# Optimization experiments

Measured on AMD Instinct MI355X. Metric: run time of the kernel, lower is better.

## Reference

```python
import jax, jax.numpy as jnp
import numpy as np

N0, N1, N2 = 120000, 40000, 10000   # sampled node counts per hop
E0, E1 = 600000, 150000             # edges per block (fanout ~15)
DIN, DH, NC = 128, 256, 47


def _glorot(k, fan_in, fan_out):
    s = (2.0 / (fan_in + fan_out)) ** 0.5
    return jax.random.normal(k, (fan_in, fan_out), jnp.float32) * s


def setup_inputs() -> dict:
    key = jax.random.key(0)
    ks = jax.random.split(key, 20)
    x0 = jax.random.normal(ks[0], (N0, DIN), jnp.float32)
    src0 = jax.random.randint(ks[1], (E0,), 0, N0)
    dst0 = jax.random.randint(ks[2], (E0,), 0, N1)
    src1 = jax.random.randint(ks[3], (E1,), 0, N1)
    dst1 = jax.random.randint(ks[4], (E1,), 0, N2)
    srcb0 = jax.random.randint(ks[5], (E0,), 0, N0)
    dstb0 = jax.random.randint(ks[6], (E0,), 0, N1)
    srcb1 = jax.random.randint(ks[7], (E1,), 0, N1)
    dstb1 = jax.random.randint(ks[8], (E1,), 0, N2)
    # id_old_value_new: must satisfy idx[:n] < n for every truncation length n,
    # i.e. idx[k] in [0, k+1)
    rng = np.random.default_rng(0)
    idx = jnp.asarray((rng.random(N0) * (np.arange(N0) + 1)).astype(np.int64))
    mix_ratio = jnp.float32(0.5)
    Wl0 = _glorot(ks[9], DIN, DH); Wr0 = _glorot(ks[10], DIN, DH)
    b0 = jnp.zeros((DH,), jnp.float32)
    Wl1 = _glorot(ks[11], DH, DH); Wr1 = _glorot(ks[12], DH, DH)
    b1 = jnp.zeros((DH,), jnp.float32)
    Wlin = _glorot(ks[13], DH, NC)
    blin = jnp.zeros((NC,), jnp.float32)
    return dict(x0=x0, src0=src0, dst0=dst0, src1=src1, dst1=dst1,
                srcb0=srcb0, dstb0=dstb0, srcb1=srcb1, dstb1=dstb1,
                idx=idx, mix_ratio=mix_ratio,
                Wl0=Wl0, Wr0=Wr0, b0=b0, Wl1=Wl1, Wr1=Wr1, b1=b1,
                Wlin=Wlin, blin=blin)


def _sage(x_all, root_x, src, dst, n_root, Wl, Wr, b):
    # PyG-style SAGEConv, mean aggregation: lin_l(mean_j x_j) + lin_r(root)
    msgs = x_all[src]                                        # [E, D] gather
    s = jax.ops.segment_sum(msgs, dst, num_segments=n_root)  # [n_root, D]
    cnt = jax.ops.segment_sum(jnp.ones_like(dst, dtype=x_all.dtype), dst,
                              num_segments=n_root)
    mean = s / jnp.maximum(cnt, 1.0)[:, None]
    return mean @ Wl + root_x @ Wr + b


def reference(x0, src0, dst0, src1, dst1, srcb0, dstb0, srcb1, dstb1,
              idx, mix_ratio, Wl0, Wr0, b0, Wl1, Wr1, b1, Wlin, blin):
    blocks = [(src0, dst0, N1), (src1, dst1, N2)]
    blocks_b = [(srcb0, dstb0, N1), (srcb1, dstb1, N2)]
    params = [(Wl0, Wr0, b0), (Wl1, Wr1, b1)]
    m = mix_ratio

    # first branch (dropout omitted: inference mode)
    aggr_xs = [x0]
    for i in range(2):
        src, dst, n_root = blocks[i]
        Wl, Wr, b = params[i]
        root_x = aggr_xs[-1][:n_root]
        x = jax.nn.relu(_sage(aggr_xs[-1], root_x, src, dst, n_root, Wl, Wr, b))
        aggr_xs.append(x)

    # permuted branch via id_old_value_new gather
    aggr_xs_b = [x[idx[: x.shape[0]]] for x in aggr_xs]

    x_mix = aggr_xs[0] * m + aggr_xs_b[0] * (1.0 - m)
    for i in range(2):
        src, dst, n_root = blocks[i]
        srcb, dstb, n_root_b = blocks_b[i]
        Wl, Wr, b = params[i]
        x_new = jax.nn.relu(_sage(aggr_xs[i], x_mix[:n_root], src, dst,
                                  n_root, Wl, Wr, b))
        x_new_b = jax.nn.relu(_sage(aggr_xs_b[i], x_mix[:n_root_b], srcb, dstb,
                                    n_root_b, Wl, Wr, b))
        x_mix = x_new * m + x_new_b * (1.0 - m)

    logits = x_mix @ Wlin + blin
    return jax.nn.log_softmax(logits, axis=-1)
```

## Files before the change

kernel.cpp:

```cpp
#include <hip/hip_runtime.h>
#include <math.h>

#define N1C 40000
#define N2C 10000
#define DIN 128
#define DH  256
#define NC  47

#define TOTCNT (2 * N1C + 2 * N2C)
#define CAP 64
#define CURSTR 16

typedef __attribute__((ext_vector_type(8))) short v8s;
typedef __attribute__((ext_vector_type(4))) float v4f;
typedef __attribute__((ext_vector_type(2))) float v2f;

#if __has_builtin(__builtin_amdgcn_cvt_pk_f32_fp8)
#define HW_FP8 1
#endif

__device__ __forceinline__ unsigned short f2bf(float f) {
    unsigned int u = __float_as_uint(f);
    u += 0x7FFF + ((u >> 16) & 1);
    return (unsigned short)(u >> 16);
}
__device__ __forceinline__ float bf2f(unsigned int h) {
    return __uint_as_float(h << 16);
}

__device__ __forceinline__ unsigned char f2e4m3(float f) {
    unsigned int u = __float_as_uint(f);
    unsigned char s = (unsigned char)((u >> 24) & 0x80);
    float a = __uint_as_float(u & 0x7FFFFFFF);
    if (a > 448.0f) a = 448.0f;
    if (a < 0.015625f) {
        int k = (int)rintf(a * 512.0f);
        return s | (unsigned char)k;
    }
    unsigned int bits = __float_as_uint(a);
    int et = (int)(bits >> 23) - 127 + 7;
    unsigned int m32 = bits & 0x7FFFFF;
    unsigned int m3 = m32 >> 20;
    unsigned int rest = m32 & 0xFFFFF;
    if (rest > 0x80000 || (rest == 0x80000 && (m3 & 1))) m3++;
    if (m3 == 8) { m3 = 0; et++; }
    if (et > 15 || (et == 15 && m3 == 7)) return s | 0x7E;
    return s | (unsigned char)((et << 3) | m3);
}

__device__ __forceinline__ void dec4(unsigned int u, float& f0, float& f1,
                                     float& f2, float& f3) {
#ifdef HW_FP8
    v2f lo = __builtin_amdgcn_cvt_pk_f32_fp8((int)u, false);
    v2f hi = __builtin_amdgcn_cvt_pk_f32_fp8((int)u, true);
    f0 = lo[0]; f1 = lo[1]; f2 = hi[0]; f3 = hi[1];
#else
    auto d1 = [](unsigned int b) -> float {
        int e = (b >> 3) & 15, mm = b & 7;
        float d = (e == 0) ? (float)mm * (1.0f / 512.0f)
                           : (1.0f + (float)mm * 0.125f) * exp2f((float)(e - 7));
        return (b & 0x80) ? -d : d;
    };
    f0 = d1(u & 0xFF); f1 = d1((u >> 8) & 0xFF);
    f2 = d1((u >> 16) & 0xFF); f3 = d1(u >> 24);
#endif
}

__global__ __launch_bounds__(256) void front_fused(
        const int* __restrict__ src0, const int* __restrict__ dst0,
        const int* __restrict__ srcb0, const int* __restrict__ dstb0,
        const int* __restrict__ src1, const int* __restrict__ dst1,
        const int* __restrict__ srcb1, const int* __restrict__ dstb1,
        const int* __restrict__ perm, int* __restrict__ cur,
        int* __restrict__ bucket, int E0, int E1, int nbFill,
        const float* __restrict__ x0, unsigned char* __restrict__ x0f,
        long n8, int nbConv,
        const float* __restrict__ Wl0, const float* __restrict__ Wr0,
        const float* __restrict__ Wl1, const float* __restrict__ Wr1,
        unsigned short* __restrict__ Wt0l, unsigned short* __restrict__ Wt0r,
        unsigned short* __restrict__ Wt1l, unsigned short* __restrict__ Wt1r) {
    int b = blockIdx.x, t = threadIdx.x;
    if (b < nbFill) {
        int e = b * 256 + t;
        int tot = 2 * E0 + 2 * E1;
        if (e >= tot) return;
        int s, bin;
        if (e < E0) {
            s = src0[e];                  bin = dst0[e];
        } else if (e < 2 * E0) {
            int le = e - E0;
            s = perm[srcb0[le]];          bin = N1C + dstb0[le];
        } else if (e < 2 * E0 + E1) {
            int le = e - 2 * E0;
            s = src1[le];                 bin = 2 * N1C + dst1[le];
        } else {
            int le = e - 2 * E0 - E1;
            s = perm[srcb1[le]];          bin = 2 * N1C + N2C + dstb1[le];
        }
        int pos = atomicAdd(&cur[(size_t)bin * CURSTR], 1);
        if (pos < CAP) bucket[(size_t)bin * CAP + pos] = s;
    } else if (b < nbFill + nbConv) {
        long i = (long)(b - nbFill) * 256 + t;
        if (i >= n8) return;
        const float4* p = (const float4*)(x0 + i * 8);
        float4 a = p[0], c = p[1];
        float f[8] = {a.x, a.y, a.z, a.w, c.x, c.y, c.z, c.w};
        unsigned int q0 = 0, q1 = 0;
#pragma unroll
        for (int j = 0; j < 8; j++) {
            unsigned int e8 = f2e4m3(f[j]);
            if (j < 4) q0 |= e8 << (8 * j); else q1 |= e8 << (8 * (j - 4));
        }
        uint2 q = {q0, q1};
        *(uint2*)(x0f + i * 8) = q;
    } else {
        int id = (b - nbFill - nbConv) * 256 + t;
        const int S0 = DIN * DH;
        const int S1 = DH * DH;
        const float* W; unsigned short* Wt; int K, loc;
        if (id < S0)                   { W = Wl0; Wt = Wt0l; K = DIN; loc = id; }
        else if (id < 2 * S0)          { W = Wr0; Wt = Wt0r; K = DIN; loc = id - S0; }
        else if (id < 2 * S0 + S1)     { W = Wl1; Wt = Wt1l; K = DH;  loc = id - 2 * S0; }
        else if (id < 2 * S0 + 2 * S1) { W = Wr1; Wt = Wt1r; K = DH;  loc = id - 2 * S0 - S1; }
        else return;
        int n = loc / K, k = loc - n * K;
        Wt[(size_t)n * K + k] = f2bf(W[(size_t)k * DH + n]);
    }
}

__global__ __launch_bounds__(256) void gather_mean_128f(
        const unsigned char* __restrict__ xf, const int* __restrict__ bucket,
        const int* __restrict__ cur, unsigned short* __restrict__ mean0,
        unsigned short* __restrict__ meanb0) {
    const int half = N1C / 8;
    int b = blockIdx.x;
    int binbase; unsigned short* outp; int rb;
    if (b < half) { binbase = 0;   outp = mean0;  rb = b; }
    else          { binbase = N1C; outp = meanb0; rb = b - half; }
    int wv = threadIdx.x >> 6, lane = threadIdx.x & 63;
    int row = rb * 8 + wv * 2 + (lane >> 5);
    int c4 = (lane & 31) * 4;
    int bin = binbase + row;
    int cnt = min(cur[(size_t)bin * CURSTR], CAP);
    const int* cs = bucket + (size_t)bin * CAP;
    float a0 = 0.0f, a1 = 0.0f, a2 = 0.0f, a3 = 0.0f;
    int i = 0;
    for (; i + 3 < cnt; i += 4) {
        int s0 = cs[i], s1 = cs[i + 1], s2 = cs[i + 2], s3 = cs[i + 3];
        unsigned int u = *(const unsigned int*)&xf[(size_t)s0 * DIN + c4];
        unsigned int v = *(const unsigned int*)&xf[(size_t)s1 * DIN + c4];
        unsigned int w = *(const unsigned int*)&xf[(size_t)s2 * DIN + c4];
        unsigned int z = *(const unsigned int*)&xf[(size_t)s3 * DIN + c4];
        float u0, u1, u2, u3, w0, w1, w2, w3, p0, p1, p2, p3, q0, q1, q2, q3;
        dec4(u, u0, u1, u2, u3);
        dec4(v, w0, w1, w2, w3);
        dec4(w, p0, p1, p2, p3);
        dec4(z, q0, q1, q2, q3);
        a0 += (u0 + w0) + (p0 + q0); a1 += (u1 + w1) + (p1 + q1);
        a2 += (u2 + w2) + (p2 + q2); a3 += (u3 + w3) + (p3 + q3);
    }
    for (; i < cnt; i++) {
        unsigned int u = *(const unsigned int*)&xf[(size_t)cs[i] * DIN + c4];
        float u0, u1, u2, u3;
        dec4(u, u0, u1, u2, u3);
        a0 += u0; a1 += u1; a2 += u2; a3 += u3;
    }
    float inv = 1.0f / (float)max(cnt, 1);
    uint2 o;
    o.x = (unsigned int)f2bf(a0 * inv) | ((unsigned int)f2bf(a1 * inv) << 16);
    o.y = (unsigned int)f2bf(a2 * inv) | ((unsigned int)f2bf(a3 * inv) << 16);
    *(uint2*)&outp[(size_t)row * DIN + c4] = o;
}

__global__ __launch_bounds__(256) void gather_mean_256f(
        const unsigned char* __restrict__ xf, const int* __restrict__ bucket,
        const int* __restrict__ cur, unsigned short* __restrict__ mean1,
        unsigned short* __restrict__ meanb1) {
    const int half = N2C / 4;
    int b = blockIdx.x;
    int binbase; unsigned short* outp; int rb;
    if (b < half) { binbase = 2 * N1C;       outp = mean1;  rb = b; }
    else          { binbase = 2 * N1C + N2C; outp = meanb1; rb = b - half; }
    int row = rb * 4 + (threadIdx.x >> 6);
    int lane = threadIdx.x & 63;
    int bin = binbase + row;
    int cnt = min(cur[(size_t)bin * CURSTR], CAP);
    const int* cs = bucket + (size_t)bin * CAP;
    float a0 = 0.0f, a1 = 0.0f, a2 = 0.0f, a3 = 0.0f;
    int i = 0;
    for (; i + 3 < cnt; i += 4) {
        int s0 = cs[i], s1 = cs[i + 1], s2 = cs[i + 2], s3 = cs[i + 3];
        unsigned int u = *(const unsigned int*)&xf[(size_t)s0 * DH + lane * 4];
        unsigned int v = *(const unsigned int*)&xf[(size_t)s1 * DH + lane * 4];
        unsigned int w = *(const unsigned int*)&xf[(size_t)s2 * DH + lane * 4];
        unsigned int z = *(const unsigned int*)&xf[(size_t)s3 * DH + lane * 4];
        float u0, u1, u2, u3, w0, w1, w2, w3, p0, p1, p2, p3, q0, q1, q2, q3;
        dec4(u, u0, u1, u2, u3);
        dec4(v, w0, w1, w2, w3);
        dec4(w, p0, p1, p2, p3);
        dec4(z, q0, q1, q2, q3);
        a0 += (u0 + w0) + (p0 + q0); a1 += (u1 + w1) + (p1 + q1);
        a2 += (u2 + w2) + (p2 + q2); a3 += (u3 + w3) + (p3 + q3);
    }
    for (; i < cnt; i++) {
        unsigned int u = *(const unsigned int*)&xf[(size_t)cs[i] * DH + lane * 4];
        float u0, u1, u2, u3;
        dec4(u, u0, u1, u2, u3);
        a0 += u0; a1 += u1; a2 += u2; a3 += u3;
    }
    float inv = 1.0f / (float)max(cnt, 1);
    uint2 o;
    o.x = (unsigned int)f2bf(a0 * inv) | ((unsigned int)f2bf(a1 * inv) << 16);
    o.y = (unsigned int)f2bf(a2 * inv) | ((unsigned int)f2bf(a3 * inv) << 16);
    *(uint2*)&outp[(size_t)row * DH + lane * 4] = o;
}

#define KP0 136
#define H0T 5
__global__ __launch_bounds__(256, 2) void hop0_mfma(
        const float* __restrict__ x0, const int* __restrict__ idx,
        const unsigned short* __restrict__ mean0, const unsigned short* __restrict__ meanb0,
        const unsigned short* __restrict__ Wtl, const unsigned short* __restrict__ Wtr,
        const float* __restrict__ b, const float* __restrict__ mixp,
        unsigned char* __restrict__ x1f, unsigned short* __restrict__ xm1) {
    __shared__ unsigned short Alds[4][16][KP0];
    int t = threadIdx.x;
    int wv = t >> 6, lane = t & 63;
    int mrow = lane & 15, quad = lane >> 4;
    float m = *mixp;

    v8s wl[4][4], wr[4][4];
    float bb[4];
#pragma unroll
    for (int ct = 0; ct < 4; ct++) {
        int n = wv * 64 + mrow * 4 + ct;
        bb[ct] = b[n];
#pragma unroll
        for (int ks = 0; ks < 4; ks++) {
            int k0 = ks * 32 + quad * 8;
            wl[ct][ks] = *(const v8s*)&Wtl[(size_t)n * DIN + k0];
            wr[ct][ks] = *(const v8s*)&Wtr[(size_t)n * DIN + k0];
        }
    }

    for (int tile = 0; tile < H0T; tile++) {
        int row0 = (blockIdx.x * H0T + tile) * 16;
        {
            int r = t >> 4, k0 = (t & 15) * 8;
            int rg = row0 + r;
            *(v8s*)&Alds[0][r][k0] = *(const v8s*)&mean0[(size_t)rg * DIN + k0];
            *(v8s*)&Alds[1][r][k0] = *(const v8s*)&meanb0[(size_t)rg * DIN + k0];
            const float4* xr4 = (const float4*)&x0[(size_t)rg * DIN + k0];
            float4 A0 = xr4[0], A1 = xr4[1];
            int ib = idx[rg];
            const float4* xb4 = (const float4*)&x0[(size_t)ib * DIN + k0];
            float4 B0 = xb4[0], B1 = xb4[1];
            float fa[8] = {A0.x, A0.y, A0.z, A0.w, A1.x, A1.y, A1.z, A1.w};
            float fb[8] = {B0.x, B0.y, B0.z, B0.w, B1.x, B1.y, B1.z, B1.w};
            v8s vr, vm;
#pragma unroll
            for (int j = 0; j < 8; j++) {
                vr[j] = (short)f2bf(fa[j]);
                vm[j] = (short)f2bf(m * fa[j] + (1.0f - m) * fb[j]);
            }
            *(v8s*)&Alds[2][r][k0] = vr;
            *(v8s*)&Alds[3][r][k0] = vm;
        }
        __syncthreads();
        v4f accA[4], accB[4], accC[4], accD[4];
#pragma unroll
        for (int ct = 0; ct < 4; ct++) {
            accA[ct] = (v4f){0.f, 0.f, 0.f, 0.f}; accB[ct] = (v4f){0.f, 0.f, 0.f, 0.f};
            accC[ct] = (v4f){0.f, 0.f, 0.f, 0.f}; accD[ct] = (v4f){0.f, 0.f, 0.f, 0.f};
        }
#pragma unroll
        for (int ks = 0; ks < 4; ks++) {
            int k0 = ks * 32 + quad * 8;
            v8s aM = *(v8s*)&Alds[0][mrow][k0];
            v8s aB = *(v8s*)&Alds[1][mrow][k0];
            v8s aR = *(v8s*)&Alds[2][mrow][k0];
            v8s aX = *(v8s*)&Alds[3][mrow][k0];
#pragma unroll
            for (int ct = 0; ct < 4; ct++) {
                accA[ct] = __builtin_amdgcn_mfma_f32_16x16x32_bf16(aM, wl[ct][ks], accA[ct], 0, 0, 0);
                accB[ct] = __builtin_amdgcn_mfma_f32_16x16x32_bf16(aB, wl[ct][ks], accB[ct], 0, 0, 0);
                accC[ct] = __builtin_amdgcn_mfma_f32_16x16x32_bf16(aR, wr[ct][ks], accC[ct], 0, 0, 0);
                accD[ct] = __builtin_amdgcn_mfma_f32_16x16x32_bf16(aX, wr[ct][ks], accD[ct], 0, 0, 0);
            }
        }
        int colb = wv * 64 + mrow * 4;
#pragma unroll
        for (int r = 0; r < 4; r++) {
            int row = row0 + quad * 4 + r;
            unsigned int xpack = 0;
            unsigned int s01, s23;
            unsigned short sh[4];
#pragma unroll
            for (int ct = 0; ct < 4; ct++) {
                float pA = accA[ct][r], pB = accB[ct][r], pC = accC[ct][r], pD = accD[ct][r];
                float xv  = fmaxf(pA + pC + bb[ct], 0.0f);
                float xn  = fmaxf(pA + pD + bb[ct], 0.0f);
                float xnb = fmaxf(pB + pD + bb[ct], 0.0f);
                xpack |= ((unsigned int)f2e4m3(xv)) << (8 * ct);
                sh[ct] = f2bf(m * xn + (1.0f - m) * xnb);
            }
            s01 = (unsigned int)sh[0] | ((unsigned int)sh[1] << 16);
            s23 = (unsigned int)sh[2] | ((unsigned int)sh[3] << 16);
            *(unsigned int*)&x1f[(size_t)row * DH + colb] = xpack;
            uint2 xm = {s01, s23};
            *(uint2*)&xm1[(size_t)row * DH + colb] = xm;
        }
        __syncthreads();
    }
}

#define KP1 264
#define H1T 2
__global__ __launch_bounds__(256, 2) void hop1_mfma(
        const unsigned short* __restrict__ mean1, const unsigned short* __restrict__ meanb1,
        const unsigned short* __restrict__ xm1,
        const unsigned short* __restrict__ Wtl, const unsigned short* __restrict__ Wtr,
        const float* __restrict__ b, const float* __restrict__ mixp,
        float* __restrict__ xm2) {
    __shared__ unsigned short Alds[3][16][KP1];
    int t = threadIdx.x;
    int wv = t >> 6, lane = t & 63;
    int mrow = lane & 15, quad = lane >> 4;
    float m = *mixp;

    v8s wlc[4][4], wrc[4][4];
    float bb[4];
#pragma unroll
    for (int ct = 0; ct < 4; ct++) {
        int n = wv * 64 + mrow * 4 + ct;
        bb[ct] = b[n];
#pragma unroll
        for (int ks = 0; ks < 4; ks++) {
            int k0 = ks * 32 + quad * 8;
            wlc[ct][ks] = *(const v8s*)&Wtl[(size_t)n * DH + k0];
            wrc[ct][ks] = *(const v8s*)&Wtr[(size_t)n * DH + k0];
        }
    }

    for (int tt = 0; tt < H1T; tt++) {
        int tIdx = blockIdx.x * H1T + tt;
        if (tIdx >= N2C / 16) break;
        int row0 = tIdx * 16;
        {
            int r = t >> 4, k0 = (t & 15) * 16;
            int rg = row0 + r;
            *(v8s*)&Alds[0][r][k0]     = *(const v8s*)&mean1[(size_t)rg * DH + k0];
            *(v8s*)&Alds[0][r][k0 + 8] = *(const v8s*)&mean1[(size_t)rg * DH + k0 + 8];
            *(v8s*)&Alds[1][r][k0]     = *(const v8s*)&meanb1[(size_t)rg * DH + k0];
            *(v8s*)&Alds[1][r][k0 + 8] = *(const v8s*)&meanb1[(size_t)rg * DH + k0 + 8];
            *(v8s*)&Alds[2][r][k0]     = *(const v8s*)&xm1[(size_t)rg * DH + k0];
            *(v8s*)&Alds[2][r][k0 + 8] = *(const v8s*)&xm1[(size_t)rg * DH + k0 + 8];
        }
        __syncthreads();
        v4f accA[4], accB[4], accC[4];
#pragma unroll
        for (int ct = 0; ct < 4; ct++) {
            accA[ct] = (v4f){0.f, 0.f, 0.f, 0.f};
            accB[ct] = (v4f){0.f, 0.f, 0.f, 0.f};
            accC[ct] = (v4f){0.f, 0.f, 0.f, 0.f};
        }
#pragma unroll
        for (int ks = 0; ks < 8; ks++) {
            int k0 = ks * 32 + quad * 8;
            v8s aM = *(v8s*)&Alds[0][mrow][k0];
            v8s aB = *(v8s*)&Alds[1][mrow][k0];
            v8s aR = *(v8s*)&Alds[2][mrow][k0];
#pragma unroll
            for (int ct = 0; ct < 4; ct++) {
                v8s bl, br;
                if (ks < 4) { bl = wlc[ct][ks]; br = wrc[ct][ks]; }
                else {
                    int n = wv * 64 + mrow * 4 + ct;
                    bl = *(const v8s*)&Wtl[(size_t)n * DH + k0];
                    br = *(const v8s*)&Wtr[(size_t)n * DH + k0];
                }
                accA[ct] = __builtin_amdgcn_mfma_f32_16x16x32_bf16(aM, bl, accA[ct], 0, 0, 0);
                accB[ct] = __builtin_amdgcn_mfma_f32_16x16x32_bf16(aB, bl, accB[ct], 0, 0, 0);
                accC[ct] = __builtin_amdgcn_mfma_f32_16x16x32_bf16(aR, br, accC[ct], 0, 0, 0);
            }
        }
        int colb = wv * 64 + mrow * 4;
#pragma unroll
        for (int r = 0; r < 4; r++) {
            int row = row0 + quad * 4 + r;
            float4 o;
            float v0 = fmaxf(accA[0][r] + accC[0][r] + bb[0], 0.0f);
            float w0 = fmaxf(accB[0][r] + accC[0][r] + bb[0], 0.0f);
            float v1 = fmaxf(accA[1][r] + accC[1][r] + bb[1], 0.0f);
            float w1 = fmaxf(accB[1][r] + accC[1][r] + bb[1], 0.0f);
            float v2 = fmaxf(accA[2][r] + accC[2][r] + bb[2], 0.0f);
            float w2 = fmaxf(accB[2][r] + accC[2][r] + bb[2], 0.0f);
            float v3 = fmaxf(accA[3][r] + accC[3][r] + bb[3], 0.0f);
            float w3 = fmaxf(accB[3][r] + accC[3][r] + bb[3], 0.0f);
            o.x = m * v0 + (1.0f - m) * w0;
            o.y = m * v1 + (1.0f - m) * w1;
            o.z = m * v2 + (1.0f - m) * w2;
            o.w = m * v3 + (1.0f - m) * w3;
            *(float4*)&xm2[(size_t)row * DH + colb] = o;
        }
        __syncthreads();
    }
}

__global__ __launch_bounds__(256) void logits_lsm(
        const float* __restrict__ xmix2, const float* __restrict__ Wlin,
        const float* __restrict__ blin, float* __restrict__ out, int nrows) {
    int w = threadIdx.x >> 6;
    int row = blockIdx.x * 4 + w;
    int t = threadIdx.x & 63;
    __shared__ float xs[4][DH];
    if (row < nrows)
        for (int i = t; i < DH; i += 64) xs[w][i] = xmix2[(size_t)row * DH + i];
    __syncthreads();
    if (row >= nrows) return;
    float acc = 0.0f;
    if (t < NC) {
        acc = blin[t];
        for (int k = 0; k < DH; k++) acc += xs[w][k] * Wlin[k * NC + t];
    }
    float v = (t < NC) ? acc : -INFINITY;
    float mx = v;
    for (int off = 32; off; off >>= 1) mx = fmaxf(mx, __shfl_xor(mx, off, 64));
    float ex = (t < NC) ? expf(acc - mx) : 0.0f;
    float sum = ex;
    for (int off = 32; off; off >>= 1) sum += __shfl_xor(sum, off, 64);
    if (t < NC) out[(size_t)row * NC + t] = acc - mx - logf(sum);
}

extern "C" void kernel_launch(void* const* d_in, const int* in_sizes, int n_in,
                              void* d_out, int out_size, void* d_ws, size_t ws_size,
                              hipStream_t stream) {
    const float* x0    = (const float*)d_in[0];
    const int*   src0  = (const int*)d_in[1];
    const int*   dst0  = (const int*)d_in[2];
    const int*   src1  = (const int*)d_in[3];
    const int*   dst1  = (const int*)d_in[4];
    const int*   srcb0 = (const int*)d_in[5];
    const int*   dstb0 = (const int*)d_in[6];
    const int*   srcb1 = (const int*)d_in[7];
    const int*   dstb1 = (const int*)d_in[8];
    const int*   idx   = (const int*)d_in[9];
    const float* mixp  = (const float*)d_in[10];
    const float* Wl0   = (const float*)d_in[11];
    const float* Wr0   = (const float*)d_in[12];
    const float* b0    = (const float*)d_in[13];
    const float* Wl1   = (const float*)d_in[14];
    const float* Wr1   = (const float*)d_in[15];
    const float* b1    = (const float*)d_in[16];
    const float* Wlin  = (const float*)d_in[17];
    const float* blin  = (const float*)d_in[18];
    float* out = (float*)d_out;

    const int E0 = in_sizes[1];
    const int E1 = in_sizes[3];
    const long x0elems = (long)in_sizes[0];

    int* wsi    = (int*)d_ws;
    int* cur    = wsi;
    int* bucket = cur + (size_t)TOTCNT * CURSTR;
    unsigned short* wsh = (unsigned short*)(bucket + (size_t)TOTCNT * CAP);
    unsigned short* mean0  = wsh;
    unsigned short* meanb0 = mean0  + (size_t)N1C * DIN;
    unsigned short* mean1  = meanb0 + (size_t)N1C * DIN;
    unsigned short* meanb1 = mean1  + (size_t)N2C * DH;
    unsigned short* xm1h   = meanb1 + (size_t)N2C * DH;
    unsigned short* Wt0l   = xm1h   + (size_t)N1C * DH;
    unsigned short* Wt0r   = Wt0l + DIN * DH;
    unsigned short* Wt1l   = Wt0r + DIN * DH;
    unsigned short* Wt1r   = Wt1l + DH * DH;
    float* xm2 = (float*)(Wt1r + DH * DH);
    unsigned char* x0f = (unsigned char*)(xm2 + (size_t)N2C * DH);
    unsigned char* x1f = x0f + (size_t)x0elems;

    hipMemsetAsync(cur, 0, sizeof(int) * (size_t)TOTCNT * CURSTR, stream);

    int etot = 2 * E0 + 2 * E1;
    int nbFill = (etot + 255) / 256;
    long n8 = x0elems / 8;
    int nbConv = (int)((n8 + 255) / 256);
    int nbW = (2 * DIN * DH + 2 * DH * DH + 255) / 256;
    front_fused<<<nbFill + nbConv + nbW, 256, 0, stream>>>(
        src0, dst0, srcb0, dstb0, src1, dst1, srcb1, dstb1, idx, cur, bucket,
        E0, E1, nbFill, x0, x0f, n8, nbConv,
        Wl0, Wr0, Wl1, Wr1, Wt0l, Wt0r, Wt1l, Wt1r);

    gather_mean_128f<<<2 * (N1C / 8), 256, 0, stream>>>(x0f, bucket, cur, mean0, meanb0);

    hop0_mfma<<<N1C / (16 * H0T), 256, 0, stream>>>(x0, idx, mean0, meanb0, Wt0l, Wt0r,
                                                    b0, mixp, x1f, xm1h);

    gather_mean_256f<<<2 * (N2C / 4), 256, 0, stream>>>(x1f, bucket, cur, mean1, meanb1);

    hop1_mfma<<<(N2C / 16 + H1T - 1) / H1T, 256, 0, stream>>>(mean1, meanb1, xm1h,
                                                              Wt1l, Wt1r, b1, mixp, xm2);

    logits_lsm<<<(N2C + 3) / 4, 256, 0, stream>>>(xm2, Wlin, blin, out, N2C);
}
```

Baseline: 341.5 us.

## Co-locate bucket counters with edge lists and use hardware FP8 packing

Moves each bin's atomic counter into the first slot of its bucket row, stride 80 ints, so counter and source list share cache lines. A small zero kernel replaces the memset of the padded counter array. The fill loop now handles two edges per thread, and software e4m3 encoding is replaced by the packed hardware fp8 convert builtin in both the x0 conversion and the hop0 epilogue. The trade-offs are a larger bucket footprint and possible rounding or saturation differences between the hardware converter and the software encoder.

```diff
diff --git a/kernel.cpp b/kernel.cpp
--- a/kernel.cpp
+++ b/kernel.cpp
@@ -9,7 +9,7 @@
 
 #define TOTCNT (2 * N1C + 2 * N2C)
 #define CAP 64
-#define CURSTR 16
+#define BSTR 80
 
 typedef __attribute__((ext_vector_type(8))) short v8s;
 typedef __attribute__((ext_vector_type(4))) float v4f;
@@ -23,9 +23,6 @@
     unsigned int u = __float_as_uint(f);
     u += 0x7FFF + ((u >> 16) & 1);
     return (unsigned short)(u >> 16);
-}
-__device__ __forceinline__ float bf2f(unsigned int h) {
-    return __uint_as_float(h << 16);
 }
 
 __device__ __forceinline__ unsigned char f2e4m3(float f) {
@@ -46,6 +43,18 @@
     if (m3 == 8) { m3 = 0; et++; }
     if (et > 15 || (et == 15 && m3 == 7)) return s | 0x7E;
     return s | (unsigned char)((et << 3) | m3);
+}
+
+__device__ __forceinline__ unsigned int pack4_e4m3(float f0, float f1,
+                                                   float f2, float f3) {
+#if __has_builtin(__builtin_amdgcn_cvt_pk_fp8_f32)
+    int q = __builtin_amdgcn_cvt_pk_fp8_f32(f0, f1, 0, false);
+    q = __builtin_amdgcn_cvt_pk_fp8_f32(f2, f3, q, true);
+    return (unsigned int)q;
+#else
+    return (unsigned int)f2e4m3(f0) | ((unsigned int)f2e4m3(f1) << 8) |
+           ((unsigned int)f2e4m3(f2) << 16) | ((unsigned int)f2e4m3(f3) << 24);
+#endif
 }
 
 __device__ __forceinline__ void dec4(unsigned int u, float& f0, float& f1,
@@ -66,13 +75,18 @@
 #endif
 }
 
+__global__ __launch_bounds__(256) void zero_counts(int* __restrict__ bucket) {
+    int i = blockIdx.x * 256 + threadIdx.x;
+    if (i < TOTCNT) bucket[(size_t)i * BSTR] = 0;
+}
+
 __global__ __launch_bounds__(256) void front_fused(
         const int* __restrict__ src0, const int* __restrict__ dst0,
         const int* __restrict__ srcb0, const int* __restrict__ dstb0,
         const int* __restrict__ src1, const int* __restrict__ dst1,
         const int* __restrict__ srcb1, const int* __restrict__ dstb1,
-        const int* __restrict__ perm, int* __restrict__ cur,
-        int* __restrict__ bucket, int E0, int E1, int nbFill,
+        const int* __restrict__ perm, int* __restrict__ bucket,
+        int E0, int E1, int nbFill,
         const float* __restrict__ x0, unsigned char* __restrict__ x0f,
         long n8, int nbConv,
         const float* __restrict__ Wl0, const float* __restrict__ Wr0,
@@ -81,37 +95,37 @@
         unsigned short* __restrict__ Wt1l, unsigned short* __restrict__ Wt1r) {
     int b = blockIdx.x, t = threadIdx.x;
     if (b < nbFill) {
-        int e = b * 256 + t;
         int tot = 2 * E0 + 2 * E1;
-        if (e >= tot) return;
-        int s, bin;
-        if (e < E0) {
-            s = src0[e];                  bin = dst0[e];
-        } else if (e < 2 * E0) {
-            int le = e - E0;
-            s = perm[srcb0[le]];          bin = N1C + dstb0[le];
-        } else if (e < 2 * E0 + E1) {
-            int le = e - 2 * E0;
-            s = src1[le];                 bin = 2 * N1C + dst1[le];
-        } else {
-            int le = e - 2 * E0 - E1;
-            s = perm[srcb1[le]];          bin = 2 * N1C + N2C + dstb1[le];
-        }
-        int pos = atomicAdd(&cur[(size_t)bin * CURSTR], 1);
-        if (pos < CAP) bucket[(size_t)bin * CAP + pos] = s;
+        int base = b * 512;
+#pragma unroll
+        for (int j = 0; j < 2; j++) {
+            int e = base + j * 256 + t;
+            if (e < tot) {
+                int s, bin;
+                if (e < E0) {
+                    s = src0[e];                  bin = dst0[e];
+                } else if (e < 2 * E0) {
+                    int le = e - E0;
+                    s = perm[srcb0[le]];          bin = N1C + dstb0[le];
+                } else if (e < 2 * E0 + E1) {
+                    int le = e - 2 * E0;
+                    s = src1[le];                 bin = 2 * N1C + dst1[le];
+                } else {
+                    int le = e - 2 * E0 - E1;
+                    s = perm[srcb1[le]];          bin = 2 * N1C + N2C + dstb1[le];
+                }
+                int pos = atomicAdd(&bucket[(size_t)bin * BSTR], 1);
+                if (pos < CAP) bucket[(size_t)bin * BSTR + 1 + pos] = s;
+            }
+        }
     } else if (b < nbFill + nbConv) {
         long i = (long)(b - nbFill) * 256 + t;
         if (i >= n8) return;
         const float4* p = (const float4*)(x0 + i * 8);
         float4 a = p[0], c = p[1];
-        float f[8] = {a.x, a.y, a.z, a.w, c.x, c.y, c.z, c.w};
-        unsigned int q0 = 0, q1 = 0;
-#pragma unroll
-        for (int j = 0; j < 8; j++) {
-            unsigned int e8 = f2e4m3(f[j]);
-            if (j < 4) q0 |= e8 << (8 * j); else q1 |= e8 << (8 * (j - 4));
-        }
-        uint2 q = {q0, q1};
+        uint2 q;
+        q.x = pack4_e4m3(a.x, a.y, a.z, a.w);
+        q.y = pack4_e4m3(c.x, c.y, c.z, c.w);
         *(uint2*)(x0f + i * 8) = q;
     } else {
         int id = (b - nbFill - nbConv) * 256 + t;
@@ -130,8 +144,7 @@
 
 __global__ __launch_bounds__(256) void gather_mean_128f(
         const unsigned char* __restrict__ xf, const int* __restrict__ bucket,
-        const int* __restrict__ cur, unsigned short* __restrict__ mean0,
-        unsigned short* __restrict__ meanb0) {
+        unsigned short* __restrict__ mean0, unsigned short* __restrict__ meanb0) {
     const int half = N1C / 8;
     int b = blockIdx.x;
     int binbase; unsigned short* outp; int rb;
@@ -141,8 +154,9 @@
     int row = rb * 8 + wv * 2 + (lane >> 5);
     int c4 = (lane & 31) * 4;
     int bin = binbase + row;
-    int cnt = min(cur[(size_t)bin * CURSTR], CAP);
-    const int* cs = bucket + (size_t)bin * CAP;
+    const int* bb = bucket + (size_t)bin * BSTR;
+    int cnt = min(bb[0], CAP);
+    const int* cs = bb + 1;
     float a0 = 0.0f, a1 = 0.0f, a2 = 0.0f, a3 = 0.0f;
     int i = 0;
     for (; i + 3 < cnt; i += 4) {
@@ -174,8 +188,7 @@
 
 __global__ __launch_bounds__(256) void gather_mean_256f(
         const unsigned char* __restrict__ xf, const int* __restrict__ bucket,
-        const int* __restrict__ cur, unsigned short* __restrict__ mean1,
-        unsigned short* __restrict__ meanb1) {
+        unsigned short* __restrict__ mean1, unsigned short* __restrict__ meanb1) {
     const int half = N2C / 4;
     int b = blockIdx.x;
     int binbase; unsigned short* outp; int rb;
@@ -184,8 +197,9 @@
     int row = rb * 4 + (threadIdx.x >> 6);
     int lane = threadIdx.x & 63;
     int bin = binbase + row;
-    int cnt = min(cur[(size_t)bin * CURSTR], CAP);
-    const int* cs = bucket + (size_t)bin * CAP;
+    const int* bb = bucket + (size_t)bin * BSTR;
+    int cnt = min(bb[0], CAP);
+    const int* cs = bb + 1;
     float a0 = 0.0f, a1 = 0.0f, a2 = 0.0f, a3 = 0.0f;
     int i = 0;
     for (; i + 3 < cnt; i += 4) {
@@ -292,20 +306,19 @@
 #pragma unroll
         for (int r = 0; r < 4; r++) {
             int row = row0 + quad * 4 + r;
-            unsigned int xpack = 0;
-            unsigned int s01, s23;
+            float xv[4];
             unsigned short sh[4];
 #pragma unroll
             for (int ct = 0; ct < 4; ct++) {
                 float pA = accA[ct][r], pB = accB[ct][r], pC = accC[ct][r], pD = accD[ct][r];
-                float xv  = fmaxf(pA + pC + bb[ct], 0.0f);
+                xv[ct]    = fmaxf(pA + pC + bb[ct], 0.0f);
                 float xn  = fmaxf(pA + pD + bb[ct], 0.0f);
                 float xnb = fmaxf(pB + pD + bb[ct], 0.0f);
-                xpack |= ((unsigned int)f2e4m3(xv)) << (8 * ct);
                 sh[ct] = f2bf(m * xn + (1.0f - m) * xnb);
             }
-            s01 = (unsigned int)sh[0] | ((unsigned int)sh[1] << 16);
-            s23 = (unsigned int)sh[2] | ((unsigned int)sh[3] << 16);
+            unsigned int xpack = pack4_e4m3(xv[0], xv[1], xv[2], xv[3]);
+            unsigned int s01 = (unsigned int)sh[0] | ((unsigned int)sh[1] << 16);
+            unsigned int s23 = (unsigned int)sh[2] | ((unsigned int)sh[3] << 16);
             *(unsigned int*)&x1f[(size_t)row * DH + colb] = xpack;
             uint2 xm = {s01, s23};
             *(uint2*)&xm1[(size_t)row * DH + colb] = xm;
@@ -461,9 +474,8 @@
     const long x0elems = (long)in_sizes[0];
 
     int* wsi    = (int*)d_ws;
-    int* cur    = wsi;
-    int* bucket = cur + (size_t)TOTCNT * CURSTR;
-    unsigned short* wsh = (unsigned short*)(bucket + (size_t)TOTCNT * CAP);
+    int* bucket = wsi;
+    unsigned short* wsh = (unsigned short*)(bucket + (size_t)TOTCNT * BSTR);
     unsigned short* mean0  = wsh;
     unsigned short* meanb0 = mean0  + (size_t)N1C * DIN;
     unsigned short* mean1  = meanb0 + (size_t)N1C * DIN;
@@ -477,24 +489,24 @@
     unsigned char* x0f = (unsigned char*)(xm2 + (size_t)N2C * DH);
     unsigned char* x1f = x0f + (size_t)x0elems;
 
-    hipMemsetAsync(cur, 0, sizeof(int) * (size_t)TOTCNT * CURSTR, stream);
+    zero_counts<<<(TOTCNT + 255) / 256, 256, 0, stream>>>(bucket);
 
     int etot = 2 * E0 + 2 * E1;
-    int nbFill = (etot + 255) / 256;
+    int nbFill = (etot + 511) / 512;
     long n8 = x0elems / 8;
     int nbConv = (int)((n8 + 255) / 256);
     int nbW = (2 * DIN * DH + 2 * DH * DH + 255) / 256;
     front_fused<<<nbFill + nbConv + nbW, 256, 0, stream>>>(
-        src0, dst0, srcb0, dstb0, src1, dst1, srcb1, dstb1, idx, cur, bucket,
+        src0, dst0, srcb0, dstb0, src1, dst1, srcb1, dstb1, idx, bucket,
         E0, E1, nbFill, x0, x0f, n8, nbConv,
         Wl0, Wr0, Wl1, Wr1, Wt0l, Wt0r, Wt1l, Wt1r);
 
-    gather_mean_128f<<<2 * (N1C / 8), 256, 0, stream>>>(x0f, bucket, cur, mean0, meanb0);
+    gather_mean_128f<<<2 * (N1C / 8), 256, 0, stream>>>(x0f, bucket, mean0, meanb0);
 
     hop0_mfma<<<N1C / (16 * H0T), 256, 0, stream>>>(x0, idx, mean0, meanb0, Wt0l, Wt0r,
                                                     b0, mixp, x1f, xm1h);
 
-    gather_mean_256f<<<2 * (N2C / 4), 256, 0, stream>>>(x1f, bucket, cur, mean1, meanb1);
+    gather_mean_256f<<<2 * (N2C / 4), 256, 0, stream>>>(x1f, bucket, mean1, meanb1);
 
     hop1_mfma<<<(N2C / 16 + H1T - 1) / H1T, 256, 0, stream>>>(mean1, meanb1, xm1h,
                                                               Wt1l, Wt1r, b1, mixp, xm2);
```

New measurement: 358.2 us. 4.9% more time.
